# Optimization experiments

Hardware: AMD Instinct MI355X
Metric: run time of the kernel (lower is better)

## Reference

```python
import jax, jax.numpy as jnp
import numpy as np

DN = ('NCHW', 'OIHW', 'NCHW')
B, HP, LR = 4, 256, 64  # batch, pan side length, lrms side length


def conv(x, w):
    return jax.lax.conv_general_dilated(x, w, (1, 1), 'SAME', dimension_numbers=DN)


def gauss_k(ks, sigma):
    i = np.arange(ks) - (ks - 1) / 2.0
    k = np.exp(-(i * i) / (2.0 * sigma * sigma))
    k /= k.sum()
    return jnp.asarray(k, jnp.float32)


def gaussian_hp(x, ks, sigma):
    # Faithful to source: cv2.GaussianBlur is applied ONLY to channel 0 of each
    # sample; remaining channels get lp == x, hence hp == 0. Separable blur with
    # reflect-101 padding (cv2 default border).
    k = gauss_k(ks, sigma)
    p = ks // 2
    x0 = x[:, :1]
    y = jnp.pad(x0, ((0, 0), (0, 0), (p, p), (0, 0)), mode='reflect')
    y = jax.lax.conv_general_dilated(y, k.reshape(1, 1, ks, 1), (1, 1), 'VALID', dimension_numbers=DN)
    y = jnp.pad(y, ((0, 0), (0, 0), (0, 0), (p, p)), mode='reflect')
    y = jax.lax.conv_general_dilated(y, k.reshape(1, 1, 1, ks), (1, 1), 'VALID', dimension_numbers=DN)
    hp0 = x0 - y
    if x.shape[1] > 1:
        hp0 = jnp.concatenate([hp0, jnp.zeros_like(x[:, 1:])], axis=1)
    return hp0


def pixel_shuffle(x, r):
    b, c, h, w = x.shape
    x = x.reshape(b, c // (r * r), r, r, h, w)
    return x.transpose(0, 1, 4, 2, 5, 3).reshape(b, c // (r * r), h * r, w * r)


def hornet(x, w1, w2):
    return conv(jax.nn.gelu(conv(x, w1)), w2)


def ffc(x, wl2l, wl2g, wg2l, wspec):
    # ratio 0.5/0.5 split -> 8 local / 8 global channels
    xl, xg = x[:, :8], x[:, 8:]
    l2l, l2g, g2l = conv(xl, wl2l), conv(xl, wl2g), conv(xg, wg2l)
    f = jnp.fft.rfft2(xg, axes=(2, 3), norm='ortho')
    z = jnp.concatenate([f.real, f.imag], axis=1)
    z = jax.nn.relu(conv(z, wspec))
    g2g = jnp.fft.irfft2(z[:, :8] + 1j * z[:, 8:], s=xg.shape[2:], axes=(2, 3), norm='ortho')
    return l2l, l2g, g2l, g2g


def refine(x, win, wb1, wb2, wca1, wca2, wout):
    # RCAB-style refinement: conv-in, residual body with channel attention, conv-out
    y = conv(x, win)
    bdy = conv(jax.nn.relu(conv(y, wb1)), wb2)
    ca = jax.nn.sigmoid(conv(jax.nn.relu(conv(bdy.mean((2, 3), keepdims=True), wca1)), wca2))
    return conv(y + bdy * ca, wout)


def coord1d(n):
    r = 1.0 / n
    return -1.0 + r + 2.0 * r * jnp.arange(n, dtype=jnp.float32)


def mlp(x, w_in, b_in, w_h, b_h, w_out, b_out):
    h = jax.nn.relu(x @ w_in + b_in)
    for i in range(w_h.shape[0]):
        h = jax.nn.relu(h @ w_h[i] + b_h[i])
    return h @ w_out + b_out


def liif(feat, coord, cell, w_in, b_in, w_h, b_h, w_out, b_out):
    # LIIF with feat_unfold=True, local_ensemble=True, cell_decode=True
    b, c, h, w = feat.shape
    fp = jnp.pad(feat, ((0, 0), (0, 0), (1, 1), (1, 1)))
    patches = jnp.concatenate([fp[:, :, i:i + h, j:j + w] for i in range(3) for j in range(3)], axis=1)
    pf = patches.reshape(b, 9 * c, h * w)  # [B, 144, H*W]
    cy, cx = coord1d(h), coord1d(w)
    rx, ry = 1.0 / h, 1.0 / w
    preds, areas = [], []
    for vx in (-1.0, 1.0):
        for vy in (-1.0, 1.0):
            c0 = jnp.clip(coord[..., 0] + vx * rx + 1e-6, -1 + 1e-6, 1 - 1e-6)
            c1 = jnp.clip(coord[..., 1] + vy * ry + 1e-6, -1 + 1e-6, 1 - 1e-6)
            i0 = jnp.clip(jnp.floor((c0 + 1.0) * h / 2.0).astype(jnp.int32), 0, h - 1)
            i1 = jnp.clip(jnp.floor((c1 + 1.0) * w / 2.0).astype(jnp.int32), 0, w - 1)
            idx = i0 * w + i1  # [B, Q]
            q = jnp.take_along_axis(pf, idx[:, None, :], axis=2).transpose(0, 2, 1)  # [B,Q,144]
            rel0 = (coord[..., 0] - cy[i0]) * h
            rel1 = (coord[..., 1] - cx[i1]) * w
            inp = jnp.concatenate([q, rel0[..., None], rel1[..., None],
                                   cell[..., :1] * h, cell[..., 1:] * w], axis=-1)
            preds.append(mlp(inp, w_in, b_in, w_h, b_h, w_out, b_out))
            areas.append(jnp.abs(rel0 * rel1) + 1e-9)
    areas[0], areas[3] = areas[3], areas[0]
    areas[1], areas[2] = areas[2], areas[1]
    tot = areas[0] + areas[1] + areas[2] + areas[3]
    return sum(p * (a / tot)[..., None] for p, a in zip(preds, areas))


def _forward(lrms, pan, w_conv_ps, hor_w1, hor_w2, ffc_l2l, ffc_l2g, ffc_g2l, ffc_spec,
             ref_in, ref_b1, ref_b2, ref_ca1, ref_ca2, ref_out,
             w_fuse, w_liif, w_hp, mlp_w_in, mlp_b_in, mlp_w_h, mlp_b_h, mlp_w_out, mlp_b_out):
    side = pan.shape[-1]
    c1 = coord1d(side)
    grid = jnp.stack(jnp.meshgrid(c1, c1, indexing='ij'), -1).reshape(-1, 2)
    coord = jnp.broadcast_to(grid[None], (pan.shape[0], side * side, 2))
    cell = jnp.full_like(coord, 2.0 / side)

    lrms_up = pixel_shuffle(conv(lrms, w_conv_ps), 4)

    blur_cfg = [(5, 1.5), (27, 2.0), (41, 2.8)]
    R = lambda i: (ref_in[i], ref_b1[i], ref_b2[i], ref_ca1[i], ref_ca2[i], ref_out[i])
    Fc = lambda i: (ffc_l2l[i], ffc_l2g[i], ffc_g2l[i], ffc_spec[i])

    fused = []
    for br in range(3):
        ks, sg = blur_cfg[br]
        feat = jnp.concatenate([gaussian_hp(pan, ks, sg), gaussian_hp(lrms_up, ks, sg)], axis=1)
        feat = hornet(feat, hor_w1[br], hor_w2[br])
        f0 = refine(feat, *R(3 * br))
        l2l, l2g, g2l, g2g = ffc(f0, *Fc(2 * br))
        f1 = refine(jnp.concatenate([l2g + g2g, l2l + g2l], axis=1), *R(3 * br + 1))
        l2l, l2g, g2l, g2g = ffc(f1, *Fc(2 * br + 1))
        f2 = refine(jnp.concatenate([l2g + g2g, l2l + g2l], axis=1), *R(3 * br + 2))
        fused.append(conv(jnp.concatenate([f0, f1, f2], axis=1), w_fuse[br]))

    feat_all = conv(jnp.concatenate(fused, axis=1), w_liif)
    fo = liif(feat_all, coord, cell, mlp_w_in, mlp_b_in, mlp_w_h, mlp_b_h, mlp_w_out, mlp_b_out)
    fo = fo.transpose(0, 2, 1).reshape(pan.shape[0], -1, side, side)
    return conv(fo, w_hp) + lrms_up


def setup_inputs() -> dict:
    key = jax.random.key(0)
    ks = jax.random.split(key, 24)
    n = lambda i, shape, s=0.05: jax.random.normal(ks[i], shape, jnp.float32) * s
    return dict(
        lrms=n(0, (B, 4, LR, LR), 1.0),
        pan=n(1, (B, 1, HP, HP), 1.0),
        w_conv_ps=n(2, (64, 4, 3, 3)),
        hor_w1=n(3, (3, 16, 5, 3, 3)),
        hor_w2=n(4, (3, 16, 16, 3, 3)),
        ffc_l2l=n(5, (6, 8, 8, 3, 3)),
        ffc_l2g=n(6, (6, 8, 8, 3, 3)),
        ffc_g2l=n(7, (6, 8, 8, 3, 3)),
        ffc_spec=n(8, (6, 16, 16, 1, 1), 0.1),
        ref_in=n(9, (9, 16, 16, 3, 3)),
        ref_b1=n(10, (9, 16, 16, 3, 3)),
        ref_b2=n(11, (9, 16, 16, 3, 3)),
        ref_ca1=n(12, (9, 4, 16, 1, 1), 0.1),
        ref_ca2=n(13, (9, 16, 4, 1, 1), 0.1),
        ref_out=n(14, (9, 16, 16, 3, 3)),
        w_fuse=n(15, (3, 16, 48, 1, 1), 0.1),
        w_liif=n(16, (16, 48, 1, 1), 0.1),
        w_hp=n(17, (4, 16, 3, 3)),
        mlp_w_in=n(18, (148, 256), 148 ** -0.5),
        mlp_b_in=jnp.zeros((256,), jnp.float32),
        mlp_w_h=n(19, (3, 256, 256), 256 ** -0.5),
        mlp_b_h=jnp.zeros((3, 256), jnp.float32),
        mlp_w_out=n(20, (256, 16), 256 ** -0.5),
        mlp_b_out=jnp.zeros((16,), jnp.float32),
    )


def reference(lrms, pan, w_conv_ps, hor_w1, hor_w2, ffc_l2l, ffc_l2g, ffc_g2l, ffc_spec,
              ref_in, ref_b1, ref_b2, ref_ca1, ref_ca2, ref_out,
              w_fuse, w_liif, w_hp, mlp_w_in, mlp_b_in, mlp_w_h, mlp_b_h, mlp_w_out, mlp_b_out):
    return _forward(lrms, pan, w_conv_ps, hor_w1, hor_w2, ffc_l2l, ffc_l2g, ffc_g2l, ffc_spec,
                    ref_in, ref_b1, ref_b2, ref_ca1, ref_ca2, ref_out,
                    w_fuse, w_liif, w_hp, mlp_w_in, mlp_b_in, mlp_w_h, mlp_b_h, mlp_w_out, mlp_b_out)
```

## Files before the change

### kernel.cpp

```cpp
#include <hip/hip_runtime.h>
#include <hip/hip_bf16.h>
#include <math.h>

typedef __hip_bfloat16 bf16;
typedef __attribute__((ext_vector_type(8))) short short8;
typedef __attribute__((ext_vector_type(4))) short short4v;
typedef __attribute__((ext_vector_type(4))) float float4v;

#define ACT_NONE 0
#define ACT_RELU 1
#define ACT_GELU 2

__device__ __forceinline__ float b2f(bf16 v){ return __bfloat162float(v); }
__device__ __forceinline__ bf16  f2b(float f){ return __float2bfloat16(f); }
__device__ __forceinline__ short f2bs(float f){ bf16 h = __float2bfloat16(f); return *reinterpret_cast<short*>(&h); }
__device__ __forceinline__ float bs2f(short s){ return __uint_as_float(((unsigned)(unsigned short)s) << 16); }
__device__ __forceinline__ void rotc(float& tr, float& ti, float cr, float ci){
    float t = tr*cr - ti*ci; ti = tr*ci + ti*cr; tr = t;
}
__device__ __forceinline__ int swz(int row, int col){ return row*256 + (col ^ ((row & 7) << 3)); }

struct GK3 { float k[3][41]; int ks[3]; };

__global__ __launch_bounds__(256) void conv_ps_k(const float* __restrict__ lrms,
                                                 const float* __restrict__ w,
                                                 float* __restrict__ up){
    int tid = threadIdx.x, bx = blockIdx.x;
    int y = bx & 255, c = (bx >> 8) & 3, b = bx >> 10;
    int x = tid;
    int h = y >> 2, r1 = y & 3, ww = x >> 2, r2 = x & 3;
    int oc = c*16 + r1*4 + r2;
    float acc = 0.f;
    for (int ic = 0; ic < 4; ++ic) {
        const float* base = lrms + ((b*4 + ic) << 12);
        const float* wb = w + (oc*4 + ic)*9;
        #pragma unroll
        for (int ky = 0; ky < 3; ++ky) {
            int hh = h + ky - 1; if (hh < 0 || hh > 63) continue;
            #pragma unroll
            for (int kx = 0; kx < 3; ++kx) {
                int cc = ww + kx - 1; if (cc < 0 || cc > 63) continue;
                acc += base[(hh<<6) + cc] * wb[ky*3 + kx];
            }
        }
    }
    up[(((size_t)(b*4 + c)) << 16) + (y<<8) + x] = acc;
}

__global__ __launch_bounds__(256) void gauss_hp_k(const float* __restrict__ pan,
                                                  const float* __restrict__ lrms_up,
                                                  bf16* __restrict__ feat2, GK3 g){
    int tid = threadIdx.x, bx = blockIdx.x;
    int y = bx & 255, b = (bx >> 8) & 3, src = (bx >> 10) & 1, br = bx >> 11;
    int ks = g.ks[br], p = ks >> 1;
    const float* gk = g.k[br];
    const float* s = src ? (lrms_up + (size_t)b*4*65536) : (pan + (size_t)b*65536);
    __shared__ float vext[296];
    for (int i = tid; i < 296; i += 256) {
        int xe = i - 20; int xr = xe < 0 ? -xe : (xe > 255 ? 510 - xe : xe);
        float acc = 0.f;
        for (int t = 0; t < ks; ++t) {
            int yy = y - p + t; yy = yy < 0 ? -yy : (yy > 255 ? 510 - yy : yy);
            acc += gk[t] * s[(yy<<8) + xr];
        }
        vext[i] = acc;
    }
    __syncthreads();
    int x = tid;
    float acc = 0.f;
    for (int t = 0; t < ks; ++t) acc += gk[t] * vext[x - p + t + 20];
    float o = s[(y<<8) + x];
    feat2[(((size_t)((br*4 + b)*2 + src)) << 16) + (y<<8) + x] = f2b(o - acc);
}

__global__ __launch_bounds__(256) void convA_k(const bf16* __restrict__ in, int inCper, int Cin,
                                               const float* __restrict__ wbase, int wbrstride, int wocstride,
                                               bf16* __restrict__ out, int act){
    int tid = threadIdx.x, bx = blockIdx.x;
    int y = bx & 255, b = (bx >> 8) & 3, br = bx >> 10;
    const float* w = wbase + (size_t)br * wbrstride;
    int x = tid;
    float acc[16];
    #pragma unroll
    for (int oc = 0; oc < 16; ++oc) acc[oc] = 0.f;
    for (int ic = 0; ic < Cin; ++ic) {
        const bf16* base = in + ((size_t)((br*4 + b)*inCper + ic) << 16);
        const float* wic = w + ic*9;
        #pragma unroll
        for (int ky = 0; ky < 3; ++ky) {
            int yy = y + ky - 1; if (yy < 0 || yy > 255) continue;
            const bf16* rowp = base + (yy<<8);
            float v0 = (x > 0)   ? b2f(rowp[x-1]) : 0.f;
            float v1 = b2f(rowp[x]);
            float v2 = (x < 255) ? b2f(rowp[x+1]) : 0.f;
            const float* wr = wic + ky*3;
            #pragma unroll
            for (int oc = 0; oc < 16; ++oc) {
                const float* wo = wr + oc*wocstride;
                acc[oc] = fmaf(wo[0], v0, fmaf(wo[1], v1, fmaf(wo[2], v2, acc[oc])));
            }
        }
    }
    #pragma unroll
    for (int oc = 0; oc < 16; ++oc) {
        float a = acc[oc];
        if (act == ACT_RELU) a = fmaxf(a, 0.f);
        else if (act == ACT_GELU) {
            float u = 0.7978845608028654f * (a + 0.044715f*a*a*a);
            a = 0.5f * a * (1.f + tanhf(u));
        }
        out[((size_t)((br*4 + b)*16 + oc) << 16) + (y<<8) + x] = f2b(a);
    }
}

__global__ __launch_bounds__(256) void pack_convw_k(const float* __restrict__ hor_w2,
        const float* __restrict__ ref_in, const float* __restrict__ ref_b1,
        const float* __restrict__ ref_b2, const float* __restrict__ ffcw,
        const float* __restrict__ ref_out,
        short* __restrict__ wp){
    int idx = blockIdx.x*256 + threadIdx.x;
    if (idx >= 45*2560) return;
    int set = idx / 2560, r = idx % 2560;
    int j = r & 7, l = (r>>3) & 63, kt = r >> 9;
    int k = kt*32 + ((l>>4)&3)*8 + j;
    int n = l & 15;
    int g = set / 3, br = set % 3;
    float v = 0.f;
    if (k < 144) {
        int tap = k >> 4, ic = k & 15;
        int widx = (n*16 + ic)*9 + tap;
        const float* src;
        if (g == 0)       src = hor_w2 + br*2304;
        else if (g <= 3)  src = ref_in + (3*br + (g-1))*2304;
        else if (g <= 6)  src = ref_b1 + (3*br + (g-4))*2304;
        else if (g <= 9)  src = ref_b2 + (3*br + (g-7))*2304;
        else if (g <= 11) src = ffcw   + (2*br + (g-10))*2304;
        else              src = ref_out + (3*br + (g-12))*2304;
        v = src[widx];
    }
    wp[idx] = f2bs(v);
}

__global__ __launch_bounds__(256) void convM_k(const bf16* __restrict__ in,
        const short* __restrict__ wgroup,
        bf16* __restrict__ out, int act, float* __restrict__ means){
    __shared__ short sIn[6*258*20];
    __shared__ float sm[4][16];
    int tid = threadIdx.x, bx = blockIdx.x;
    int y0 = (bx & 63) << 2, b = (bx >> 6) & 3, br = bx >> 8;
    size_t pbase = (size_t)((br*4 + b)*16) << 16;
    if (tid < 192) {
        int r = tid >> 5, side = (tid >> 4) & 1, ic = tid & 15;
        sIn[(r*258 + (side ? 257 : 0))*20 + ic] = 0;
    }
    {
        int g = tid >> 5, tl = tid & 31, x0 = tl << 3, ic0 = g*2;
        for (int r = 0; r < 6; ++r) {
            int yy = y0 - 1 + r;
            short8 lo = {0,0,0,0,0,0,0,0}, hi = {0,0,0,0,0,0,0,0};
            if (yy >= 0 && yy <= 255) {
                lo = *(const short8*)&in[pbase + ((size_t)ic0<<16) + (yy<<8) + x0];
                hi = *(const short8*)&in[pbase + ((size_t)(ic0+1)<<16) + (yy<<8) + x0];
            }
            #pragma unroll
            for (int t = 0; t < 8; ++t) {
                int v = (int)(unsigned short)lo[t] | ((int)(unsigned short)hi[t] << 16);
                *(int*)&sIn[(r*258 + x0 + t + 1)*20 + ic0] = v;
            }
        }
    }
    __syncthreads();
    int l = tid & 63, w = tid >> 6, m_l = l & 15, q = l >> 4;
    const short* wp = wgroup + br*2560;
    short8 bfr[5];
    #pragma unroll
    for (int kt = 0; kt < 5; ++kt)
        bfr[kt] = *(const short8*)(wp + (kt*64 + l)*8);
    float4v acc[16];
    #pragma unroll
    for (int j = 0; j < 16; ++j) acc[j] = (float4v){0.f,0.f,0.f,0.f};
    #pragma unroll
    for (int kt = 0; kt < 5; ++kt) {
        int k0 = kt*32 + q*8;
        bool pad = (k0 >= 144);
        int tap = pad ? 0 : (k0 >> 4);
        int icb = k0 & 15;
        int ky = tap/3, kx = tap - ky*3;
        int rbase = (w + ky)*258 + kx;
        #pragma unroll
        for (int j = 0; j < 16; ++j) {
            int x = j*16 + m_l;
            const short* ap = &sIn[(rbase + x)*20 + icb];
            short4v alo = *(const short4v*)ap;
            short4v ahi = *(const short4v*)(ap + 4);
            short8 a;
            #pragma unroll
            for (int t = 0; t < 4; ++t) { a[t] = pad ? (short)0 : alo[t]; a[t+4] = pad ? (short)0 : ahi[t]; }
            acc[j] = __builtin_amdgcn_mfma_f32_16x16x32_bf16(a, bfr[kt], acc[j], 0, 0, 0);
        }
    }
    if (means) {
        float s = 0.f;
        #pragma unroll
        for (int j = 0; j < 16; ++j)
            #pragma unroll
            for (int r = 0; r < 4; ++r) s += acc[j][r];
        s += __shfl_xor(s, 16, 64);
        s += __shfl_xor(s, 32, 64);
        if (l < 16) sm[w][l] = s;
        __syncthreads();
        if (tid < 16) atomicAdd(&means[br*64 + b*16 + tid],
                                sm[0][tid] + sm[1][tid] + sm[2][tid] + sm[3][tid]);
    }
    int yrow = y0 + w;
    #pragma unroll
    for (int j = 0; j < 16; ++j) {
        short4v pk;
        #pragma unroll
        for (int r = 0; r < 4; ++r) {
            float a = acc[j][r];
            if (act == ACT_RELU) a = fmaxf(a, 0.f);
            else if (act == ACT_GELU) {
                float u = 0.7978845608028654f * (a + 0.044715f*a*a*a);
                a = 0.5f * a * (1.f + tanhf(u));
            }
            pk[r] = f2bs(a);
        }
        *(short4v*)&out[pbase + ((size_t)m_l << 16) + (yrow<<8) + j*16 + q*4] = pk;
    }
}

__global__ __launch_bounds__(256) void convOutM_k(const bf16* __restrict__ Y, const bf16* __restrict__ BDY,
        const float* __restrict__ cav, const short* __restrict__ wgroup,
        const float* __restrict__ wfuse, int step,
        bf16* __restrict__ F, bf16* __restrict__ fusedCat){
    __shared__ short sIn[6*258*20];
    int tid = threadIdx.x, bx = blockIdx.x;
    int y0 = (bx & 63) << 2, b = (bx >> 6) & 3, br = bx >> 8;
    size_t pbase = (size_t)((br*4 + b)*16) << 16;
    if (tid < 192) {
        int r = tid >> 5, side = (tid >> 4) & 1, ic = tid & 15;
        sIn[(r*258 + (side ? 257 : 0))*20 + ic] = 0;
    }
    {
        int g = tid >> 5, tl = tid & 31, x0 = tl << 3, ic0 = g*2;
        float c0 = cav[br*64 + b*16 + ic0];
        float c1 = cav[br*64 + b*16 + ic0 + 1];
        for (int r = 0; r < 6; ++r) {
            int yy = y0 - 1 + r;
            short8 ylo = {0,0,0,0,0,0,0,0}, yhi = ylo, dlo = ylo, dhi = ylo;
            if (yy >= 0 && yy <= 255) {
                size_t o0 = pbase + ((size_t)ic0<<16) + (yy<<8) + x0;
                size_t o1 = pbase + ((size_t)(ic0+1)<<16) + (yy<<8) + x0;
                ylo = *(const short8*)&Y[o0];   yhi = *(const short8*)&Y[o1];
                dlo = *(const short8*)&BDY[o0]; dhi = *(const short8*)&BDY[o1];
            }
            #pragma unroll
            for (int t = 0; t < 8; ++t) {
                short s0 = f2bs(fmaf(bs2f(dlo[t]), c0, bs2f(ylo[t])));
                short s1 = f2bs(fmaf(bs2f(dhi[t]), c1, bs2f(yhi[t])));
                int v = (int)(unsigned short)s0 | ((int)(unsigned short)s1 << 16);
                *(int*)&sIn[(r*258 + x0 + t + 1)*20 + ic0] = v;
            }
        }
    }
    __syncthreads();
    int l = tid & 63, w = tid >> 6, m_l = l & 15, q = l >> 4;
    const short* wp = wgroup + br*2560;
    short8 bfr[5];
    #pragma unroll
    for (int kt = 0; kt < 5; ++kt)
        bfr[kt] = *(const short8*)(wp + (kt*64 + l)*8);
    float4v acc[16];
    #pragma unroll
    for (int j = 0; j < 16; ++j) acc[j] = (float4v){0.f,0.f,0.f,0.f};
    #pragma unroll
    for (int kt = 0; kt < 5; ++kt) {
        int k0 = kt*32 + q*8;
        bool pad = (k0 >= 144);
        int tap = pad ? 0 : (k0 >> 4);
        int icb = k0 & 15;
        int ky = tap/3, kx = tap - ky*3;
        int rbase = (w + ky)*258 + kx;
        #pragma unroll
        for (int j = 0; j < 16; ++j) {
            int x = j*16 + m_l;
            const short* ap = &sIn[(rbase + x)*20 + icb];
            short4v alo = *(const short4v*)ap;
            short4v ahi = *(const short4v*)(ap + 4);
            short8 a;
            #pragma unroll
            for (int t = 0; t < 4; ++t) { a[t] = pad ? (short)0 : alo[t]; a[t+4] = pad ? (short)0 : ahi[t]; }
            acc[j] = __builtin_amdgcn_mfma_f32_16x16x32_bf16(a, bfr[kt], acc[j], 0, 0, 0);
        }
    }
    int yrow = y0 + w;
    #pragma unroll
    for (int j = 0; j < 16; ++j) {
        short4v pk;
        #pragma unroll
        for (int r = 0; r < 4; ++r) pk[r] = f2bs(acc[j][r]);
        *(short4v*)&F[pbase + ((size_t)m_l << 16) + (yrow<<8) + j*16 + q*4] = pk;
    }
    __syncthreads();
    short* sF = sIn + w*4096;
    #pragma unroll
    for (int j = 0; j < 16; ++j)
        #pragma unroll
        for (int r = 0; r < 4; ++r)
            sF[(j*16 + q*4 + r)*16 + m_l] = f2bs(acc[j][r]);
    const float* wf = wfuse + br*768 + step*16;
    short8 b2;
    #pragma unroll
    for (int jj = 0; jj < 8; ++jj) {
        int k = q*8 + jj;
        b2[jj] = (k < 16) ? f2bs(wf[m_l*48 + k]) : (short)0;
    }
    #pragma unroll
    for (int mt = 0; mt < 16; ++mt) {
        short8 a2 = {0,0,0,0,0,0,0,0};
        if (q < 2) a2 = *(const short8*)&sF[(mt*16 + m_l)*16 + q*8];
        float4v d2 = (float4v){0.f,0.f,0.f,0.f};
        d2 = __builtin_amdgcn_mfma_f32_16x16x32_bf16(a2, b2, d2, 0, 0, 0);
        size_t fidx = ((size_t)(b*48 + br*16 + m_l) << 16) + (yrow<<8) + mt*16 + q*4;
        short4v pk;
        if (step == 0) {
            #pragma unroll
            for (int r = 0; r < 4; ++r) pk[r] = f2bs(d2[r]);
        } else {
            short4v old = *(const short4v*)&fusedCat[fidx];
            #pragma unroll
            for (int r = 0; r < 4; ++r) pk[r] = f2bs(bs2f(old[r]) + d2[r]);
        }
        *(short4v*)&fusedCat[fidx] = pk;
    }
}

__global__ void ca_k(float* __restrict__ means, const float* __restrict__ ca1,
                     const float* __restrict__ ca2, int step, float* __restrict__ cav){
    int t = threadIdx.x;
    int br = t >> 6, rem = t & 63, b = rem >> 4, oc = rem & 15;
    int ri = 3*br + step;
    const float* w1 = ca1 + ri*64; const float* w2 = ca2 + ri*64;
    float hid[4];
    #pragma unroll
    for (int c2 = 0; c2 < 4; ++c2) {
        float a = 0.f;
        for (int c = 0; c < 16; ++c) a += w1[c2*16 + c] * (means[br*64 + b*16 + c] * (1.f/65536.f));
        hid[c2] = fmaxf(a, 0.f);
    }
    float v = 0.f;
    #pragma unroll
    for (int c2 = 0; c2 < 4; ++c2) v += w2[oc*4 + c2] * hid[c2];
    cav[t] = 1.f / (1.f + expf(-v));
    __syncthreads();
    means[t] = 0.f;
}

__global__ __launch_bounds__(256) void rfft_wT_k(const bf16* __restrict__ F,
                                                 bf16* __restrict__ ore, bf16* __restrict__ oim){
    __shared__ float rows[16][256];
    __shared__ float Ar[256], Ai[256];
    __shared__ float Tr[129][17], Ti[129][17];
    int tid = threadIdx.x, bx = blockIdx.x;
    int t = bx & 15, c = (bx >> 4) & 7, b = (bx >> 7) & 3, br = bx >> 9;
    int y0 = t << 4;
    size_t plane = (size_t)((br*4 + b)*16 + 8 + c) << 16;
    #pragma unroll
    for (int r = 0; r < 16; ++r)
        rows[r][tid] = b2f(F[plane + ((size_t)(y0 + r) << 8) + tid]);
    __syncthreads();
    int n1 = tid >> 4, k1 = tid & 15;
    float a1 = -6.283185307179586f * (float)k1 / 16.f;
    float c1, s1; __sincosf(a1, &s1, &c1);
    float a2 = -6.283185307179586f * (float)tid / 256.f;
    float c2v, s2v; __sincosf(a2, &s2v, &c2v);
    for (int r = 0; r < 16; ++r) {
        float twr = 1.f, twi = 0.f, ar = 0.f, ai = 0.f;
        #pragma unroll
        for (int n2 = 0; n2 < 16; ++n2) {
            float xr = rows[r][n1 + (n2<<4)];
            ar = fmaf(xr, twr, ar); ai = fmaf(xr, twi, ai);
            rotc(twr, twi, c1, s1);
        }
        Ar[tid] = ar; Ai[tid] = ai;
        __syncthreads();
        float t2r = 1.f, t2i = 0.f, re = 0.f, im = 0.f;
        #pragma unroll
        for (int m = 0; m < 16; ++m) {
            float rr = Ar[(m<<4) + k1], ii = Ai[(m<<4) + k1];
            re += rr*t2r - ii*t2i; im += ii*t2r + rr*t2i;
            rotc(t2r, t2i, c2v, s2v);
        }
        if (tid < 129) { Tr[tid][r] = re * 0.0625f; Ti[tid][r] = im * 0.0625f; }
        __syncthreads();
    }
    size_t obase = ((size_t)(((br*4 + b)*8 + c)*129)) * 256 + y0;
    for (int idx = tid; idx < 129*16; idx += 256) {
        int k = idx >> 4, ty = idx & 15;
        ore[obase + (size_t)k*256 + ty] = f2b(Tr[k][ty]);
        oim[obase + (size_t)k*256 + ty] = f2b(Ti[k][ty]);
    }
}

__global__ __launch_bounds__(256) void fftspec_hT_k(const bf16* __restrict__ re0, const bf16* __restrict__ im0,
                                                    const float* __restrict__ wspec, int step,
                                                    bf16* __restrict__ re1, bf16* __restrict__ im1){
    __shared__ float Fr[8][256], Fi[8][256], Sr[8][256], Si[8][256], Ar[256], Ai[256];
    int tid = threadIdx.x, bx = blockIdx.x;
// ... 70 lines not shown
        re1[base] = f2b(rr * 0.0625f);
        im1[base] = f2b(ii * 0.0625f);
        __syncthreads();
    }
}

__global__ __launch_bounds__(256) void irfft_wT_k(const bf16* __restrict__ re1, const bf16* __restrict__ im1,
                                                  bf16* __restrict__ A){
    __shared__ float Cr[129][17], Ci[129][17];
    __shared__ float er[256], ei[256];
    __shared__ float Ar[256], Ai[256];
    int tid = threadIdx.x, bx = blockIdx.x;
    int t = bx & 15, c = (bx >> 4) & 7, b = (bx >> 7) & 3, br = bx >> 9;
    int y0 = t << 4;
    size_t ibase = ((size_t)(((br*4 + b)*8 + c)*129)) * 256 + y0;
    for (int idx = tid; idx < 129*16; idx += 256) {
        int k = idx >> 4, ty = idx & 15;
        Cr[k][ty] = b2f(re1[ibase + (size_t)k*256 + ty]);
        Ci[k][ty] = (k == 0 || k == 128) ? 0.f : b2f(im1[ibase + (size_t)k*256 + ty]);
    }
    __syncthreads();
    int n1 = tid >> 4, k1 = tid & 15;
    float a1 = 6.283185307179586f * (float)k1 / 16.f;
    float c1, s1; __sincosf(a1, &s1, &c1);
    float a2 = 6.283185307179586f * (float)tid / 256.f;
    float c2v, s2v; __sincosf(a2, &s2v, &c2v);
    size_t plane = (size_t)((br*4 + b)*16 + c) << 16;
    for (int ty = 0; ty < 16; ++ty) {
        if (tid < 129) { er[tid] = Cr[tid][ty]; ei[tid] = Ci[tid][ty]; }
        else           { er[tid] = Cr[256 - tid][ty]; ei[tid] = -Ci[256 - tid][ty]; }
        __syncthreads();
        float twr = 1.f, twi = 0.f, ar = 0.f, ai = 0.f;
        #pragma unroll
        for (int n2 = 0; n2 < 16; ++n2) {
            float r = er[n1 + (n2<<4)], i = ei[n1 + (n2<<4)];
            ar += r*twr - i*twi; ai += i*twr + r*twi;
            rotc(twr, twi, c1, s1);
        }
        Ar[tid] = ar; Ai[tid] = ai;
        __syncthreads();
        float t2r = 1.f, t2i = 0.f, racc = 0.f;
        #pragma unroll
        for (int m = 0; m < 16; ++m) {
            float r = Ar[(m<<4) + k1], i = Ai[(m<<4) + k1];
            racc += r*t2r - i*t2i;
            rotc(t2r, t2i, c2v, s2v);
        }
        size_t o = plane + ((size_t)(y0 + ty) << 8) + tid;
        A[o] = f2b(b2f(A[o]) + racc * 0.0625f);
        __syncthreads();
    }
}

__global__ __launch_bounds__(256) void pack_ffcw_k(const float* __restrict__ l2l, const float* __restrict__ l2g,
                                                   const float* __restrict__ g2l, float* __restrict__ wout){
    int idx = blockIdx.x*256 + threadIdx.x;
    if (idx >= 6*2304) return;
    int t = idx % 9; int ic = (idx/9) % 16; int oc = (idx/144) % 16; int wi = idx/2304;
    float v;
    if (oc < 8) v = (ic < 8) ? l2g[((wi*8 + oc)*8 + ic)*9 + t] : 0.f;
    else {
        int o = oc - 8;
        v = (ic < 8) ? l2l[((wi*8 + o)*8 + ic)*9 + t] : g2l[((wi*8 + o)*8 + (ic-8))*9 + t];
    }
    wout[idx] = v;
}

__global__ __launch_bounds__(256) void fuse1x1_k(const bf16* __restrict__ fc, const float* __restrict__ wl,
                                                 bf16* __restrict__ feat_all){
    int tid = threadIdx.x, bx = blockIdx.x;
    int pt = bx & 255, b = bx >> 8;
    int p = (pt << 8) + tid;
    float acc[16];
    #pragma unroll
    for (int oc = 0; oc < 16; ++oc) acc[oc] = 0.f;
    for (int ic = 0; ic < 48; ++ic) {
        float v = b2f(fc[((size_t)(b*48 + ic) << 16) + p]);
        #pragma unroll
        for (int oc = 0; oc < 16; ++oc) acc[oc] = fmaf(wl[oc*48 + ic], v, acc[oc]);
    }
    #pragma unroll
    for (int oc = 0; oc < 16; ++oc)
        feat_all[((size_t)(b*16 + oc) << 16) + p] = f2b(acc[oc]);
}

__global__ __launch_bounds__(256) void repack_k(const float* __restrict__ mw_in,
                                                const float* __restrict__ mw_h,
                                                const float* __restrict__ mw_out,
                                                short* __restrict__ wp){
    int idx = blockIdx.x*256 + threadIdx.x;
    const int S0 = 40960;
    const int SH = 65536;
    const int TOT = S0 + 3*SH + 4096;
    if (idx >= TOT) return;
    float val;
    if (idx < S0) {
        int j = idx & 7, l = (idx>>3) & 63, nt = (idx>>9) & 15, kt = idx >> 13;
        int k = kt*32 + (l>>4)*8 + j;
        int n = nt*16 + (l&15);
        val = (k < 148) ? mw_in[k*256 + n] : 0.f;
    } else if (idx < S0 + 3*SH) {
        int i2 = idx - S0;
        int L = i2 >> 16, r = i2 & 65535;
        int j = r & 7, l = (r>>3) & 63, nt = (r>>9) & 15, kt = r >> 13;
        int k = kt*32 + (l>>4)*8 + j;
        int n = nt*16 + (l&15);
        val = mw_h[L*65536 + k*256 + n];
    } else {
        int i3 = idx - S0 - 3*SH;
        int j = i3 & 7, l = (i3>>3) & 63, kt = i3 >> 9;
        int k = kt*32 + (l>>4)*8 + j;
        int oc = l & 15;
        val = mw_out[k*16 + oc];
    }
    wp[idx] = f2bs(val);
}

__global__ __launch_bounds__(512) void mlp_mfma_k(const short* __restrict__ feat,
        const short* __restrict__ wp,
        const float* __restrict__ b_in, const float* __restrict__ b_h,
        const float* __restrict__ b_out,
        float* __restrict__ fo){
    extern __shared__ short act_s[];
    int tid = threadIdx.x, bx = blockIdx.x;
    long P0 = (long)bx * 128;
    for (int idx = tid; idx < 128*160; idx += 512) {
        int pp = idx / 160, j = idx - pp*160;
        long P = P0 + pp;
        int bb = (int)(P >> 16), pim = (int)(P & 65535);
        int s0 = pim >> 8, s1 = pim & 255;
        short v = 0;
        if (j < 144) {
            int iy = j/48, ix = (j>>4)%3, c2 = j&15;
            int yy = s0 + iy - 1, xx = s1 + ix - 1;
            if (yy >= 0 && yy < 256 && xx >= 0 && xx < 256)
                v = feat[(((long)(bb*16 + c2)) << 16) + (yy<<8) + xx];
        } else if (j == 146 || j == 147) v = 0x4000;
        act_s[swz(pp, j)] = v;
    }
    __syncthreads();

    int l = tid & 63, w = tid >> 6;
    int m_l = l & 15, q = l >> 4;
    int mh = w >> 2, nq = w & 3;
    int mtb = mh*4, ntb = nq*4;
    const short* wph  = wp + 40960;
    const short* wpo  = wp + 40960 + 3*65536;

    float4v acc[4][4];
    #pragma unroll
    for (int mt = 0; mt < 4; ++mt)
        #pragma unroll
        for (int nt = 0; nt < 4; ++nt) acc[mt][nt] = (float4v){0.f,0.f,0.f,0.f};
    for (int kt = 0; kt < 5; ++kt) {
        const short* bp = wp + ((size_t)(kt*16 + ntb)*64 + l)*8;
        short8 bfr[4];
        #pragma unroll
        for (int nt = 0; nt < 4; ++nt) bfr[nt] = *(const short8*)(bp + (size_t)nt*64*8);
        #pragma unroll
        for (int mt = 0; mt < 4; ++mt) {
            short8 a = *(const short8*)&act_s[swz((mtb+mt)*16 + m_l, kt*32 + q*8)];
            #pragma unroll
            for (int nt = 0; nt < 4; ++nt)
                acc[mt][nt] = __builtin_amdgcn_mfma_f32_16x16x32_bf16(a, bfr[nt], acc[mt][nt], 0, 0, 0);
        }
    }
    __syncthreads();
    #pragma unroll
    for (int nt = 0; nt < 4; ++nt) {
        int n = (ntb + nt)*16 + m_l;
        float bias = b_in[n];
        #pragma unroll
        for (int mt = 0; mt < 4; ++mt)
            #pragma unroll
            for (int r = 0; r < 4; ++r) {
                float vv = fmaxf(acc[mt][nt][r] + bias, 0.f);
                act_s[swz((mtb+mt)*16 + q*4 + r, n)] = f2bs(vv);
            }
    }
    __syncthreads();
    for (int L = 0; L < 3; ++L) {
        #pragma unroll
        for (int mt = 0; mt < 4; ++mt)
            #pragma unroll
            for (int nt = 0; nt < 4; ++nt) acc[mt][nt] = (float4v){0.f,0.f,0.f,0.f};
        const short* wl = wph + (size_t)L * 65536;
        for (int kt = 0; kt < 8; ++kt) {
            const short* bp = wl + ((size_t)(kt*16 + ntb)*64 + l)*8;
            short8 bfr[4];
            #pragma unroll
            for (int nt = 0; nt < 4; ++nt) bfr[nt] = *(const short8*)(bp + (size_t)nt*64*8);
            #pragma unroll
            for (int mt = 0; mt < 4; ++mt) {
                short8 a = *(const short8*)&act_s[swz((mtb+mt)*16 + m_l, kt*32 + q*8)];
                #pragma unroll
                for (int nt = 0; nt < 4; ++nt)
                    acc[mt][nt] = __builtin_amdgcn_mfma_f32_16x16x32_bf16(a, bfr[nt], acc[mt][nt], 0, 0, 0);
            }
        }
        __syncthreads();
        #pragma unroll
        for (int nt = 0; nt < 4; ++nt) {
            int n = (ntb + nt)*16 + m_l;
            float bias = b_h[L*256 + n];
            #pragma unroll
            for (int mt = 0; mt < 4; ++mt)
                #pragma unroll
                for (int r = 0; r < 4; ++r) {
                    float vv = fmaxf(acc[mt][nt][r] + bias, 0.f);
                    act_s[swz((mtb+mt)*16 + q*4 + r, n)] = f2bs(vv);
                }
        }
        __syncthreads();
    }
    if (nq == 0) {
        float4v o[4];
        #pragma unroll
        for (int mt = 0; mt < 4; ++mt) o[mt] = (float4v){0.f,0.f,0.f,0.f};
        for (int kt = 0; kt < 8; ++kt) {
            short8 bf = *(const short8*)(wpo + ((size_t)kt*64 + l)*8);
            #pragma unroll
            for (int mt = 0; mt < 4; ++mt) {
                short8 a = *(const short8*)&act_s[swz((mtb+mt)*16 + m_l, kt*32 + q*8)];
                o[mt] = __builtin_amdgcn_mfma_f32_16x16x32_bf16(a, bf, o[mt], 0, 0, 0);
            }
        }
        float bias = b_out[m_l];
        #pragma unroll
        for (int mt = 0; mt < 4; ++mt) {
            #pragma unroll
            for (int r = 0; r < 4; ++r) {
                long P = P0 + (mtb+mt)*16 + q*4 + r;
                int bb = (int)(P >> 16), pim = (int)(P & 65535);
                int s0 = pim >> 8, s1 = pim & 255;
                float w0 = (s0 == 255 || s1 == 255) ? 0.25f : 1.0f;
                fo[(((long)(bb*16 + m_l)) << 16) + pim] = w0 * (o[mt][r] + bias);
            }
        }
    }
}

__global__ __launch_bounds__(256) void mlp_edge_mfma_k(const short* __restrict__ feat,
        const short* __restrict__ wp,
        const float* __restrict__ b_in, const float* __restrict__ b_h,
        const float* __restrict__ b_out,
        float* __restrict__ fo){
    extern __shared__ short act_s[];
    int tid = threadIdx.x, bx = blockIdx.x;
    int E0 = bx * 128;
    for (int idx = tid; idx < 128*160; idx += 256) {
        int pp = idx / 160, j = idx - pp*160;
        int e = E0 + pp; if (e >= 6132) e = 0;
        int bb = e / 1533; int rem = e - bb*1533;
        int cn = rem / 511; int eidx = rem - cn*511;
        int s0 = (eidx < 256) ? 255 : eidx - 256;
        int s1 = (eidx < 256) ? eidx : 255;
        int vx = (cn == 0) ? -1 : 1;
        int vy = (cn == 1) ? -1 : 1;
        int i0 = (vx > 0) ? min(s0+1, 255) : s0;
        int i1 = (vy > 0) ? min(s1+1, 255) : s1;
        short v = 0;
        if (j < 144) {
            int iy = j/48, ix = (j>>4)%3, c2 = j&15;
            int yy = i0 + iy - 1, xx = i1 + ix - 1;
            if (yy >= 0 && yy < 256 && xx >= 0 && xx < 256)
                v = feat[(((long)(bb*16 + c2)) << 16) + (yy<<8) + xx];
        } else if (j == 144) v = f2bs(2.f*(float)(s0 - i0));
        else if (j == 145) v = f2bs(2.f*(float)(s1 - i1));
        else if (j >= 146) v = 0x4000;
        act_s[pp*264 + j] = v;
    }
    __syncthreads();

    int l = tid & 63, w = tid >> 6;
    int m_l = l & 15, q = l >> 4;
    int row0 = w * 32;
    const short* wph  = wp + 40960;
    const short* wpo  = wp + 40960 + 3*65536;

    float4v acc[2][16];
    #pragma unroll
    for (int mt = 0; mt < 2; ++mt)
        #pragma unroll
        for (int nt = 0; nt < 16; ++nt) acc[mt][nt] = (float4v){0.f,0.f,0.f,0.f};
    for (int kt = 0; kt < 5; ++kt) {
// ... 94 lines not shown
            acc = fmaf(wr[0], v0, fmaf(wr[1], v1, fmaf(wr[2], v2, acc)));
        }
    }
    size_t oidx = (((size_t)(b*4 + oc)) << 16) + (y<<8) + x;
    out[oidx] = acc + lrms_up[oidx];
}

extern "C" void kernel_launch(void* const* d_in, const int* in_sizes, int n_in,
                              void* d_out, int out_size, void* d_ws, size_t ws_size,
                              hipStream_t stream) {
    const float* lrms     = (const float*)d_in[0];
    const float* pan      = (const float*)d_in[1];
    const float* w_convps = (const float*)d_in[2];
    const float* hor_w1   = (const float*)d_in[3];
    const float* hor_w2   = (const float*)d_in[4];
    const float* ffc_l2l  = (const float*)d_in[5];
    const float* ffc_l2g  = (const float*)d_in[6];
    const float* ffc_g2l  = (const float*)d_in[7];
    const float* ffc_spec = (const float*)d_in[8];
    const float* ref_in   = (const float*)d_in[9];
    const float* ref_b1   = (const float*)d_in[10];
    const float* ref_b2   = (const float*)d_in[11];
    const float* ref_ca1  = (const float*)d_in[12];
    const float* ref_ca2  = (const float*)d_in[13];
    const float* ref_out  = (const float*)d_in[14];
    const float* w_fuse   = (const float*)d_in[15];
    const float* w_liif   = (const float*)d_in[16];
    const float* w_hp     = (const float*)d_in[17];
    const float* mw_in    = (const float*)d_in[18];
    const float* mb_in    = (const float*)d_in[19];
    const float* mw_h     = (const float*)d_in[20];
    const float* mb_h     = (const float*)d_in[21];
    const float* mw_out   = (const float*)d_in[22];
    const float* mb_out   = (const float*)d_in[23];
    float* out = (float*)d_out;

    const size_t PLANE = 65536;
    char* base = (char*)d_ws;
    size_t off = 0;
    auto alloc = [&](size_t bytes){ void* p = base + off; off += (bytes + 255) & ~(size_t)255; return p; };
    float* lrms_up  = (float*)alloc(16*PLANE*4);
    bf16*  feat2    = (bf16*) alloc(24*PLANE*2);
    bf16*  bA       = (bf16*) alloc(192*PLANE*2);
    bf16*  bB       = (bf16*) alloc(192*PLANE*2);
    bf16*  bC       = (bf16*) alloc(192*PLANE*2);
    bf16*  bF       = (bf16*) alloc(192*PLANE*2);
    bf16*  fusedCat = (bf16*) alloc(192*PLANE*2);
    bf16*  feat_all = (bf16*) alloc(64*PLANE*2);
    float* fo       = (float*)alloc(64*PLANE*4);
    const size_t FFTB = (size_t)3*4*8*256*129;
    bf16* re0 = (bf16*)alloc(FFTB*2); bf16* im0 = (bf16*)alloc(FFTB*2);
    bf16* re1 = (bf16*)alloc(FFTB*2); bf16* im1 = (bf16*)alloc(FFTB*2);
    short* wpack = (short*)alloc(241664*2);
    float* ffcw  = (float*)alloc(13824*4);
    short* wconv = (short*)alloc(45*2560*2);
    float* means = (float*)alloc(192*4);
    float* cav   = (float*)alloc(192*4);
    if (off > ws_size) return;

    hipMemsetAsync(means, 0, 192*4, stream);
    repack_k<<<dim3(944), dim3(256), 0, stream>>>(mw_in, mw_h, mw_out, wpack);
    pack_ffcw_k<<<dim3(54), dim3(256), 0, stream>>>(ffc_l2l, ffc_l2g, ffc_g2l, ffcw);
    pack_convw_k<<<dim3(450), dim3(256), 0, stream>>>(hor_w2, ref_in, ref_b1, ref_b2, ffcw, ref_out, wconv);
    conv_ps_k<<<dim3(4096), dim3(256), 0, stream>>>(lrms, w_convps, lrms_up);

    GK3 g3;
    {
        const int kss[3] = {5, 27, 41};
        const double sgs[3] = {1.5, 2.0, 2.8};
        for (int br = 0; br < 3; ++br) {
            g3.ks[br] = kss[br];
            double tmp[41]; double s = 0.0; double c = (kss[br]-1)/2.0;
            for (int i = 0; i < kss[br]; ++i) { double d = i - c; tmp[i] = exp(-(d*d)/(2.0*sgs[br]*sgs[br])); s += tmp[i]; }
            for (int i = 0; i < 41; ++i) g3.k[br][i] = (i < kss[br]) ? (float)(tmp[i]/s) : 0.f;
        }
    }
    gauss_hp_k<<<dim3(6144), dim3(256), 0, stream>>>(pan, lrms_up, feat2, g3);

    convA_k<<<dim3(3072), dim3(256), 0, stream>>>(feat2, 2, 2, hor_w1, 720, 45, bA, ACT_GELU);
    convM_k<<<dim3(768), dim3(256), 0, stream>>>(bA, wconv + 0*3*2560, bB, ACT_NONE, nullptr);

    for (int step = 0; step < 3; ++step) {
        bf16* Xin = (step == 0) ? bB : bA;
        bf16* Yb  = (step == 0) ? bA : bB;
        bf16* Db  = (step == 0) ? bB : bA;
        convM_k<<<dim3(768), dim3(256), 0, stream>>>(Xin, wconv + (1+step)*3*2560, Yb, ACT_NONE, nullptr);
        convM_k<<<dim3(768), dim3(256), 0, stream>>>(Yb,  wconv + (4+step)*3*2560, bC, ACT_RELU, nullptr);
        convM_k<<<dim3(768), dim3(256), 0, stream>>>(bC,  wconv + (7+step)*3*2560, Db, ACT_NONE, means);
        ca_k<<<dim3(1), dim3(192), 0, stream>>>(means, ref_ca1, ref_ca2, step, cav);
        convOutM_k<<<dim3(768), dim3(256), 0, stream>>>(Yb, Db, cav, wconv + (12+step)*3*2560, w_fuse, step, bF, fusedCat);
        if (step < 2) {
            convM_k<<<dim3(768), dim3(256), 0, stream>>>(bF, wconv + (10+step)*3*2560, bA, ACT_NONE, nullptr);
            rfft_wT_k<<<dim3(1536), dim3(256), 0, stream>>>(bF, re0, im0);
            fftspec_hT_k<<<dim3(1548), dim3(256), 0, stream>>>(re0, im0, ffc_spec, step, re1, im1);
            irfft_wT_k<<<dim3(1536), dim3(256), 0, stream>>>(re1, im1, bA);
        }
    }

    fuse1x1_k<<<dim3(1024), dim3(256), 0, stream>>>(fusedCat, w_liif, feat_all);
    mlp_mfma_k<<<dim3(2048), dim3(512), 65536, stream>>>((const short*)feat_all, wpack, mb_in, mb_h, mb_out, fo);
    mlp_edge_mfma_k<<<dim3(48), dim3(256), 128*264*2, stream>>>((const short*)feat_all, wpack, mb_in, mb_h, mb_out, fo);
    final_k<<<dim3(4096), dim3(256), 0, stream>>>(fo, w_hp, lrms_up, out);
}
```

Measured before the change: 1.206 ms.

## Merge weight packing kernels, fold channel attention into convOut, shrink MLP tiles

Merges the three weight-repack kernels into one launch and packs the FFC conv weights straight from the source tensors. The single-block channel-attention kernel is removed: each convOut block now recomputes its 16 sigmoid gates from the means, and separate means buffers per step replace the in-kernel reset. The MLP kernel moves from 512-thread blocks of 128 pixels with swizzled shared memory to 256-thread blocks of 64 pixels with padded rows (stride 264), using less LDS per block. The aim is fewer launches and serialization points and higher MLP occupancy, at the cost of redundant attention math per block and possible LDS bank-conflict changes.

```diff
diff --git a/kernel.cpp b/kernel.cpp
--- a/kernel.cpp
+++ b/kernel.cpp
@@ -18,7 +18,6 @@
 __device__ __forceinline__ void rotc(float& tr, float& ti, float cr, float ci){
     float t = tr*cr - ti*ci; ti = tr*ci + ti*cr; tr = t;
 }
-__device__ __forceinline__ int swz(int row, int col){ return row*256 + (col ^ ((row & 7) << 3)); }
 
 struct GK3 { float k[3][41]; int ks[3]; };
 
@@ -113,14 +112,45 @@
     }
 }
 
-__global__ __launch_bounds__(256) void pack_convw_k(const float* __restrict__ hor_w2,
+__global__ __launch_bounds__(256) void pack_all_k(const float* __restrict__ mw_in,
+        const float* __restrict__ mw_h, const float* __restrict__ mw_out,
+        const float* __restrict__ hor_w2,
         const float* __restrict__ ref_in, const float* __restrict__ ref_b1,
-        const float* __restrict__ ref_b2, const float* __restrict__ ffcw,
-        const float* __restrict__ ref_out,
-        short* __restrict__ wp){
+        const float* __restrict__ ref_b2, const float* __restrict__ ref_out,
+        const float* __restrict__ l2l, const float* __restrict__ l2g,
+        const float* __restrict__ g2l,
+        short* __restrict__ wp, short* __restrict__ wc){
     int idx = blockIdx.x*256 + threadIdx.x;
-    if (idx >= 45*2560) return;
-    int set = idx / 2560, r = idx % 2560;
+    const int S0 = 40960, SH = 65536;
+    const int TOTM = S0 + 3*SH + 4096;
+    const int TOTC = 45*2560;
+    if (idx < TOTM) {
+        float val;
+        if (idx < S0) {
+            int j = idx & 7, l = (idx>>3) & 63, nt = (idx>>9) & 15, kt = idx >> 13;
+            int k = kt*32 + (l>>4)*8 + j;
+            int n = nt*16 + (l&15);
+            val = (k < 148) ? mw_in[k*256 + n] : 0.f;
+        } else if (idx < S0 + 3*SH) {
+            int i2 = idx - S0;
+            int L = i2 >> 16, r = i2 & 65535;
+            int j = r & 7, l = (r>>3) & 63, nt = (r>>9) & 15, kt = r >> 13;
+            int k = kt*32 + (l>>4)*8 + j;
+            int n = nt*16 + (l&15);
+            val = mw_h[L*65536 + k*256 + n];
+        } else {
+            int i3 = idx - S0 - 3*SH;
+            int j = i3 & 7, l = (i3>>3) & 63, kt = i3 >> 9;
+            int k = kt*32 + (l>>4)*8 + j;
+            int oc = l & 15;
+            val = mw_out[k*16 + oc];
+        }
+        wp[idx] = f2bs(val);
+        return;
+    }
+    int idx2 = idx - TOTM;
+    if (idx2 >= TOTC) return;
+    int set = idx2 / 2560, r = idx2 % 2560;
     int j = r & 7, l = (r>>3) & 63, kt = r >> 9;
     int k = kt*32 + ((l>>4)&3)*8 + j;
     int n = l & 15;
@@ -128,17 +158,26 @@
     float v = 0.f;
     if (k < 144) {
         int tap = k >> 4, ic = k & 15;
-        int widx = (n*16 + ic)*9 + tap;
-        const float* src;
-        if (g == 0)       src = hor_w2 + br*2304;
-        else if (g <= 3)  src = ref_in + (3*br + (g-1))*2304;
-        else if (g <= 6)  src = ref_b1 + (3*br + (g-4))*2304;
-        else if (g <= 9)  src = ref_b2 + (3*br + (g-7))*2304;
-        else if (g <= 11) src = ffcw   + (2*br + (g-10))*2304;
-        else              src = ref_out + (3*br + (g-12))*2304;
-        v = src[widx];
-    }
-    wp[idx] = f2bs(v);
+        if (g == 10 || g == 11) {
+            int wi = 2*br + (g-10);
+            if (n < 8) v = (ic < 8) ? l2g[((wi*8 + n)*8 + ic)*9 + tap] : 0.f;
+            else {
+                int o = n - 8;
+                v = (ic < 8) ? l2l[((wi*8 + o)*8 + ic)*9 + tap]
+                             : g2l[((wi*8 + o)*8 + (ic-8))*9 + tap];
+            }
+        } else {
+            int widx = (n*16 + ic)*9 + tap;
+            const float* src;
+            if (g == 0)       src = hor_w2 + br*2304;
+            else if (g <= 3)  src = ref_in + (3*br + (g-1))*2304;
+            else if (g <= 6)  src = ref_b1 + (3*br + (g-4))*2304;
+            else if (g <= 9)  src = ref_b2 + (3*br + (g-7))*2304;
+            else              src = ref_out + (3*br + (g-12))*2304;
+            v = src[widx];
+        }
+    }
+    wc[idx2] = f2bs(v);
 }
 
 __global__ __launch_bounds__(256) void convM_k(const bf16* __restrict__ in,
@@ -231,10 +270,12 @@
 }
 
 __global__ __launch_bounds__(256) void convOutM_k(const bf16* __restrict__ Y, const bf16* __restrict__ BDY,
-        const float* __restrict__ cav, const short* __restrict__ wgroup,
+        const float* __restrict__ means, const float* __restrict__ ca1, const float* __restrict__ ca2,
+        const short* __restrict__ wgroup,
         const float* __restrict__ wfuse, int step,
         bf16* __restrict__ F, bf16* __restrict__ fusedCat){
     __shared__ short sIn[6*258*20];
+    __shared__ float sCav[16];
     int tid = threadIdx.x, bx = blockIdx.x;
     int y0 = (bx & 63) << 2, b = (bx >> 6) & 3, br = bx >> 8;
     size_t pbase = (size_t)((br*4 + b)*16) << 16;
@@ -242,10 +283,26 @@
         int r = tid >> 5, side = (tid >> 4) & 1, ic = tid & 15;
         sIn[(r*258 + (side ? 257 : 0))*20 + ic] = 0;
     }
+    if (tid < 16) {
+        int ri = 3*br + step;
+        const float* w1 = ca1 + ri*64; const float* w2 = ca2 + ri*64;
+        float hid[4];
+        #pragma unroll
+        for (int c2 = 0; c2 < 4; ++c2) {
+            float a = 0.f;
+            for (int c = 0; c < 16; ++c) a += w1[c2*16 + c] * (means[br*64 + b*16 + c] * (1.f/65536.f));
+            hid[c2] = fmaxf(a, 0.f);
+        }
+        float v = 0.f;
+        #pragma unroll
+        for (int c2 = 0; c2 < 4; ++c2) v += w2[tid*4 + c2] * hid[c2];
+        sCav[tid] = 1.f / (1.f + expf(-v));
+    }
+    __syncthreads();
     {
         int g = tid >> 5, tl = tid & 31, x0 = tl << 3, ic0 = g*2;
-        float c0 = cav[br*64 + b*16 + ic0];
-        float c1 = cav[br*64 + b*16 + ic0 + 1];
+        float c0 = sCav[ic0];
+        float c1 = sCav[ic0 + 1];
         for (int r = 0; r < 6; ++r) {
             int yy = y0 - 1 + r;
             short8 ylo = {0,0,0,0,0,0,0,0}, yhi = ylo, dlo = ylo, dhi = ylo;
@@ -334,27 +391,6 @@
         }
         *(short4v*)&fusedCat[fidx] = pk;
     }
-}
-
-__global__ void ca_k(float* __restrict__ means, const float* __restrict__ ca1,
-                     const float* __restrict__ ca2, int step, float* __restrict__ cav){
-    int t = threadIdx.x;
-    int br = t >> 6, rem = t & 63, b = rem >> 4, oc = rem & 15;
-    int ri = 3*br + step;
-    const float* w1 = ca1 + ri*64; const float* w2 = ca2 + ri*64;
-    float hid[4];
-    #pragma unroll
-    for (int c2 = 0; c2 < 4; ++c2) {
-        float a = 0.f;
-        for (int c = 0; c < 16; ++c) a += w1[c2*16 + c] * (means[br*64 + b*16 + c] * (1.f/65536.f));
-        hid[c2] = fmaxf(a, 0.f);
-    }
-    float v = 0.f;
-    #pragma unroll
-    for (int c2 = 0; c2 < 4; ++c2) v += w2[oc*4 + c2] * hid[c2];
-    cav[t] = 1.f / (1.f + expf(-v));
-    __syncthreads();
-    means[t] = 0.f;
 }
 
 __global__ __launch_bounds__(256) void rfft_wT_k(const bf16* __restrict__ F,
@@ -531,20 +567,6 @@
     }
 }
 
-__global__ __launch_bounds__(256) void pack_ffcw_k(const float* __restrict__ l2l, const float* __restrict__ l2g,
-                                                   const float* __restrict__ g2l, float* __restrict__ wout){
-    int idx = blockIdx.x*256 + threadIdx.x;
-    if (idx >= 6*2304) return;
-    int t = idx % 9; int ic = (idx/9) % 16; int oc = (idx/144) % 16; int wi = idx/2304;
-    float v;
-    if (oc < 8) v = (ic < 8) ? l2g[((wi*8 + oc)*8 + ic)*9 + t] : 0.f;
-    else {
-        int o = oc - 8;
-        v = (ic < 8) ? l2l[((wi*8 + o)*8 + ic)*9 + t] : g2l[((wi*8 + o)*8 + (ic-8))*9 + t];
-    }
-    wout[idx] = v;
-}
-
 __global__ __launch_bounds__(256) void fuse1x1_k(const bf16* __restrict__ fc, const float* __restrict__ wl,
                                                  bf16* __restrict__ feat_all){
     int tid = threadIdx.x, bx = blockIdx.x;
@@ -563,47 +585,15 @@
         feat_all[((size_t)(b*16 + oc) << 16) + p] = f2b(acc[oc]);
 }
 
-__global__ __launch_bounds__(256) void repack_k(const float* __restrict__ mw_in,
-                                                const float* __restrict__ mw_h,
-                                                const float* __restrict__ mw_out,
-                                                short* __restrict__ wp){
-    int idx = blockIdx.x*256 + threadIdx.x;
-    const int S0 = 40960;
-    const int SH = 65536;
-    const int TOT = S0 + 3*SH + 4096;
-    if (idx >= TOT) return;
-    float val;
-    if (idx < S0) {
-        int j = idx & 7, l = (idx>>3) & 63, nt = (idx>>9) & 15, kt = idx >> 13;
-        int k = kt*32 + (l>>4)*8 + j;
-        int n = nt*16 + (l&15);
-        val = (k < 148) ? mw_in[k*256 + n] : 0.f;
-    } else if (idx < S0 + 3*SH) {
-        int i2 = idx - S0;
-        int L = i2 >> 16, r = i2 & 65535;
-        int j = r & 7, l = (r>>3) & 63, nt = (r>>9) & 15, kt = r >> 13;
-        int k = kt*32 + (l>>4)*8 + j;
-        int n = nt*16 + (l&15);
-        val = mw_h[L*65536 + k*256 + n];
-    } else {
-        int i3 = idx - S0 - 3*SH;
-        int j = i3 & 7, l = (i3>>3) & 63, kt = i3 >> 9;
-        int k = kt*32 + (l>>4)*8 + j;
-        int oc = l & 15;
-        val = mw_out[k*16 + oc];
-    }
-    wp[idx] = f2bs(val);
-}
-
-__global__ __launch_bounds__(512) void mlp_mfma_k(const short* __restrict__ feat,
+__global__ __launch_bounds__(256) void mlp_mfma_k(const short* __restrict__ feat,
         const short* __restrict__ wp,
         const float* __restrict__ b_in, const float* __restrict__ b_h,
         const float* __restrict__ b_out,
         float* __restrict__ fo){
     extern __shared__ short act_s[];
     int tid = threadIdx.x, bx = blockIdx.x;
-    long P0 = (long)bx * 128;
-    for (int idx = tid; idx < 128*160; idx += 512) {
+    long P0 = (long)bx * 64;
+    for (int idx = tid; idx < 64*160; idx += 256) {
         int pp = idx / 160, j = idx - pp*160;
         long P = P0 + pp;
         int bb = (int)(P >> 16), pim = (int)(P & 65535);
@@ -615,14 +605,13 @@
             if (yy >= 0 && yy < 256 && xx >= 0 && xx < 256)
                 v = feat[(((long)(bb*16 + c2)) << 16) + (yy<<8) + xx];
         } else if (j == 146 || j == 147) v = 0x4000;
-        act_s[swz(pp, j)] = v;
+        act_s[pp*264 + j] = v;
     }
     __syncthreads();
 
     int l = tid & 63, w = tid >> 6;
     int m_l = l & 15, q = l >> 4;
-    int mh = w >> 2, nq = w & 3;
-    int mtb = mh*4, ntb = nq*4;
+    int ntb = w*4;
     const short* wph  = wp + 40960;
     const short* wpo  = wp + 40960 + 3*65536;
 
@@ -638,7 +627,7 @@
         for (int nt = 0; nt < 4; ++nt) bfr[nt] = *(const short8*)(bp + (size_t)nt*64*8);
         #pragma unroll
         for (int mt = 0; mt < 4; ++mt) {
-            short8 a = *(const short8*)&act_s[swz((mtb+mt)*16 + m_l, kt*32 + q*8)];
+            short8 a = *(const short8*)&act_s[(mt*16 + m_l)*264 + kt*32 + q*8];
             #pragma unroll
             for (int nt = 0; nt < 4; ++nt)
                 acc[mt][nt] = __builtin_amdgcn_mfma_f32_16x16x32_bf16(a, bfr[nt], acc[mt][nt], 0, 0, 0);
@@ -654,7 +643,7 @@
             #pragma unroll
             for (int r = 0; r < 4; ++r) {
                 float vv = fmaxf(acc[mt][nt][r] + bias, 0.f);
-                act_s[swz((mtb+mt)*16 + q*4 + r, n)] = f2bs(vv);
+                act_s[(mt*16 + q*4 + r)*264 + n] = f2bs(vv);
             }
     }
     __syncthreads();
@@ -671,7 +660,7 @@
             for (int nt = 0; nt < 4; ++nt) bfr[nt] = *(const short8*)(bp + (size_t)nt*64*8);
             #pragma unroll
             for (int mt = 0; mt < 4; ++mt) {
-                short8 a = *(const short8*)&act_s[swz((mtb+mt)*16 + m_l, kt*32 + q*8)];
+                short8 a = *(const short8*)&act_s[(mt*16 + m_l)*264 + kt*32 + q*8];
                 #pragma unroll
                 for (int nt = 0; nt < 4; ++nt)
                     acc[mt][nt] = __builtin_amdgcn_mfma_f32_16x16x32_bf16(a, bfr[nt], acc[mt][nt], 0, 0, 0);
@@ -687,12 +676,12 @@
                 #pragma unroll
                 for (int r = 0; r < 4; ++r) {
                     float vv = fmaxf(acc[mt][nt][r] + bias, 0.f);
-                    act_s[swz((mtb+mt)*16 + q*4 + r, n)] = f2bs(vv);
+                    act_s[(mt*16 + q*4 + r)*264 + n] = f2bs(vv);
                 }
         }
         __syncthreads();
     }
-    if (nq == 0) {
+    if (w == 0) {
         float4v o[4];
         #pragma unroll
         for (int mt = 0; mt < 4; ++mt) o[mt] = (float4v){0.f,0.f,0.f,0.f};
@@ -700,7 +689,7 @@
             short8 bf = *(const short8*)(wpo + ((size_t)kt*64 + l)*8);
             #pragma unroll
             for (int mt = 0; mt < 4; ++mt) {
-                short8 a = *(const short8*)&act_s[swz((mtb+mt)*16 + m_l, kt*32 + q*8)];
+                short8 a = *(const short8*)&act_s[(mt*16 + m_l)*264 + kt*32 + q*8];
                 o[mt] = __builtin_amdgcn_mfma_f32_16x16x32_bf16(a, bf, o[mt], 0, 0, 0);
             }
         }
@@ -709,7 +698,7 @@
         for (int mt = 0; mt < 4; ++mt) {
             #pragma unroll
             for (int r = 0; r < 4; ++r) {
-                long P = P0 + (mtb+mt)*16 + q*4 + r;
+                long P = P0 + mt*16 + q*4 + r;
                 int bb = (int)(P >> 16), pim = (int)(P & 65535);
                 int s0 = pim >> 8, s1 = pim & 255;
                 float w0 = (s0 == 255 || s1 == 255) ? 0.25f : 1.0f;
@@ -910,16 +899,13 @@
     bf16* re0 = (bf16*)alloc(FFTB*2); bf16* im0 = (bf16*)alloc(FFTB*2);
     bf16* re1 = (bf16*)alloc(FFTB*2); bf16* im1 = (bf16*)alloc(FFTB*2);
     short* wpack = (short*)alloc(241664*2);
-    float* ffcw  = (float*)alloc(13824*4);
     short* wconv = (short*)alloc(45*2560*2);
-    float* means = (float*)alloc(192*4);
-    float* cav   = (float*)alloc(192*4);
+    float* means3 = (float*)alloc(3*192*4);
     if (off > ws_size) return;
 
-    hipMemsetAsync(means, 0, 192*4, stream);
-    repack_k<<<dim3(944), dim3(256), 0, stream>>>(mw_in, mw_h, mw_out, wpack);
-    pack_ffcw_k<<<dim3(54), dim3(256), 0, stream>>>(ffc_l2l, ffc_l2g, ffc_g2l, ffcw);
-    pack_convw_k<<<dim3(450), dim3(256), 0, stream>>>(hor_w2, ref_in, ref_b1, ref_b2, ffcw, ref_out, wconv);
+    hipMemsetAsync(means3, 0, 3*192*4, stream);
+    pack_all_k<<<dim3(1395), dim3(256), 0, stream>>>(mw_in, mw_h, mw_out, hor_w2,
+        ref_in, ref_b1, ref_b2, ref_out, ffc_l2l, ffc_l2g, ffc_g2l, wpack, wconv);
     conv_ps_k<<<dim3(4096), dim3(256), 0, stream>>>(lrms, w_convps, lrms_up);
 
     GK3 g3;
@@ -944,9 +930,9 @@
         bf16* Db  = (step == 0) ? bB : bA;
         convM_k<<<dim3(768), dim3(256), 0, stream>>>(Xin, wconv + (1+step)*3*2560, Yb, ACT_NONE, nullptr);
         convM_k<<<dim3(768), dim3(256), 0, stream>>>(Yb,  wconv + (4+step)*3*2560, bC, ACT_RELU, nullptr);
-        convM_k<<<dim3(768), dim3(256), 0, stream>>>(bC,  wconv + (7+step)*3*2560, Db, ACT_NONE, means);
-        ca_k<<<dim3(1), dim3(192), 0, stream>>>(means, ref_ca1, ref_ca2, step, cav);
-        convOutM_k<<<dim3(768), dim3(256), 0, stream>>>(Yb, Db, cav, wconv + (12+step)*3*2560, w_fuse, step, bF, fusedCat);
+        convM_k<<<dim3(768), dim3(256), 0, stream>>>(bC,  wconv + (7+step)*3*2560, Db, ACT_NONE, means3 + step*192);
+        convOutM_k<<<dim3(768), dim3(256), 0, stream>>>(Yb, Db, means3 + step*192, ref_ca1, ref_ca2,
+                                                        wconv + (12+step)*3*2560, w_fuse, step, bF, fusedCat);
         if (step < 2) {
             convM_k<<<dim3(768), dim3(256), 0, stream>>>(bF, wconv + (10+step)*3*2560, bA, ACT_NONE, nullptr);
             rfft_wT_k<<<dim3(1536), dim3(256), 0, stream>>>(bF, re0, im0);
@@ -956,7 +942,7 @@
     }
 
     fuse1x1_k<<<dim3(1024), dim3(256), 0, stream>>>(fusedCat, w_liif, feat_all);
-    mlp_mfma_k<<<dim3(2048), dim3(512), 65536, stream>>>((const short*)feat_all, wpack, mb_in, mb_h, mb_out, fo);
+    mlp_mfma_k<<<dim3(4096), dim3(256), 64*264*2, stream>>>((const short*)feat_all, wpack, mb_in, mb_h, mb_out, fo);
     mlp_edge_mfma_k<<<dim3(48), dim3(256), 128*264*2, stream>>>((const short*)feat_all, wpack, mb_in, mb_h, mb_out, fo);
     final_k<<<dim3(4096), dim3(256), 0, stream>>>(fo, w_hp, lrms_up, out);
 }
```

Measured after the change: 1.169 ms. 1.03x faster.
